# Performance work log

Hardware: AMD Instinct MI355X
Metric: run time of the kernel (lower is better)

The kernel has to match this reference:

```python
import jax, jax.numpy as jnp
import numpy as np

ALPHA = 0.3

def setup_inputs() -> dict:
    key = jax.random.key(0)
    k1, k2, k3, k4 = jax.random.split(key, 4)
    bz, sl, n_pos = 64, 1024, 50
    a_arc = jax.random.normal(k1, (bz, sl, sl), dtype=jnp.float32)
    s_arc = jax.random.normal(k2, (bz, sl, sl), dtype=jnp.float32)
    adds = jax.random.randint(k3, (bz, sl), 0, n_pos, dtype=jnp.int32)
    pos = jax.random.randint(k4, (bz, sl), 0, n_pos, dtype=jnp.int32)
    return {"a_arc": a_arc, "s_arc": s_arc, "adds": adds, "pos": pos, "n_pos": n_pos}


def reference(a_arc, s_arc, adds, pos, n_pos):
    # Bin index for every (head, dep) pair: bin = adds[b,i]*n_pos + adds[b,j]
    bins_add = adds[:, :, None] * n_pos + adds[:, None, :]          # [bz, sl, sl] int32
    # Histogram: sum a_arc values per POS-pair bin (replaces the O(n_pos^2) masked loop)
    score_arc = jax.ops.segment_sum(
        a_arc.reshape(-1), bins_add.reshape(-1), num_segments=n_pos * n_pos)
    score_arc = jax.nn.sigmoid(score_arc)                            # [n_pos^2]
    # Broadcast the binned scores back onto s_arc via the pos-pair bins
    bins_pos = pos[:, :, None] * n_pos + pos[:, None, :]             # [bz, sl, sl]
    return s_arc + ALPHA * score_arc[bins_pos]
```

## Files before the change

### kernel.cpp

```cpp
#include <hip/hip_runtime.h>

constexpr int NPOS  = 50;
constexpr int NBINS = NPOS * NPOS;
constexpr int SL    = 1024;
constexpr int BZ    = 64;
constexpr float ALPHA = 0.3f;

constexpr int NRNG      = 8;
constexpr int PSLICE    = 352;
constexpr int H_THREADS = 256;
constexpr int H_BLOCKS  = BZ * NRNG;

__device__ __forceinline__ int rng_lo(int r) { return r < 2 ? 7 * r : 14 + 6 * (r - 2); }
__device__ __forceinline__ int rng_sz(int r) { return r < 2 ? 7 : 6; }

constexpr int R2_THREADS = 256;
constexpr int R2_BLOCKS  = (NBINS + R2_THREADS - 1) / R2_THREADS;
constexpr int A_THREADS      = 256;
constexpr int ROWS_PER_BLOCK = 32;
constexpr int BLOCKS_PER_B   = SL / ROWS_PER_BLOCK;
constexpr int A_BLOCKS       = BZ * BLOCKS_PER_B;

__global__ __launch_bounds__(H_THREADS) void hist_gather(
    const float* __restrict__ a, const int* __restrict__ adds,
    float* __restrict__ g_part) {
  __shared__ int   adds_s[SL];
  __shared__ float accL[8][SL];
  __shared__ int   list[SL + 8];
  __shared__ int   order2[SL];
  __shared__ int   cnt8[8], off8[8];
  __shared__ int   cntQ[NPOS], offQs[NPOS], offQm[NPOS];
  __shared__ int   nrows_s;

  const int tid = threadIdx.x;
  const int b   = blockIdx.x / NRNG;
  const int rg  = blockIdx.x % NRNG;
  const int lo  = rng_lo(rg), sz = rng_sz(rg);

  ((int4*)adds_s)[tid] = ((const int4*)(adds + (size_t)b * SL))[tid];
  #pragma unroll
  for (int p = 0; p < 8; ++p) ((float4*)&accL[p][0])[tid] = float4{0, 0, 0, 0};
  if (tid < 8) cnt8[tid] = 0;
  if (tid < NPOS) cntQ[tid] = 0;
  __syncthreads();

  for (int i = tid; i < SL; i += H_THREADS) {
    const int p = adds_s[i];
    const int pl = p - lo;
    if ((unsigned)pl < (unsigned)sz) atomicAdd(&cnt8[pl], 1);
    atomicAdd(&cntQ[p], 1);
  }
  __syncthreads();
  if (tid == 0) {
    int run = 0;
    #pragma unroll
    for (int c = 0; c < 8; ++c) { off8[c] = run; run += cnt8[c]; }
    nrows_s = run;
  } else if (tid == 64) {
    int run = 0;
    for (int c = 0; c < NPOS; ++c) { offQs[c] = run; offQm[c] = run; run += cntQ[c]; }
  }
  __syncthreads();
  for (int i = tid; i < SL; i += H_THREADS) {
    const int p = adds_s[i];
    const int pl = p - lo;
    if ((unsigned)pl < (unsigned)sz)
      list[atomicAdd(&off8[pl], 1)] = (pl << 12) | i;
    order2[atomicAdd(&offQm[p], 1)] = i;
  }
  __syncthreads();
  const int N    = nrows_s;
  const int Npad = (N + 7) & ~7;
  if (tid < 8 && N + tid < Npad)
    list[N + tid] = (7 << 12) | (N > 0 ? (list[N - 1] & 0xFFF) : 0);
  __syncthreads();

  const float4* __restrict__ Ab = (const float4*)(a + (size_t)b * SL * SL);
  float4 creg = {0, 0, 0, 0};
  int pcur = 7;

  int    eA[8], eB[8];
  float4 vA[8], vB[8];
  auto loadbank = [&](int (&e)[8], float4 (&v)[8], int k) {
    #pragma unroll
    for (int u = 0; u < 8; ++u) {
      e[u] = __builtin_amdgcn_readfirstlane(list[k + u]);
      v[u] = Ab[(size_t)(e[u] & 0xFFF) * (SL / 4) + tid];
    }
  };
  auto procbank = [&](int (&e)[8], float4 (&v)[8]) {
    #pragma unroll
    for (int u = 0; u < 8; ++u) {
      const int pl = e[u] >> 12;
      if (pl != pcur) {
        ((float4*)&accL[pcur][0])[tid] = creg;
        creg = float4{0, 0, 0, 0};
        pcur = pl;
      }
      creg.x += v[u].x; creg.y += v[u].y; creg.z += v[u].z; creg.w += v[u].w;
    }
  };

  if (Npad > 0) {
    pcur = list[0] >> 12;
    loadbank(eA, vA, 0);
    for (int k = 0; k < Npad; k += 16) {
      if (k + 8 < Npad) loadbank(eB, vB, k + 8);
      procbank(eA, vA);
      if (k + 16 < Npad) loadbank(eA, vA, k + 16);
      if (k + 8 < Npad) procbank(eB, vB);
    }
    ((float4*)&accL[pcur][0])[tid] = creg;
  }
  __syncthreads();

  float* __restrict__ gp = g_part + (size_t)blockIdx.x * PSLICE;
  for (int bin = tid; bin < sz * NPOS; bin += H_THREADS) {
    const int pl = bin / NPOS, q = bin % NPOS;
    const int s0 = offQs[q], n = cntQ[q];
    float s = 0.0f;
    for (int k2 = 0; k2 < n; ++k2) s += accL[pl][order2[s0 + k2]];
    gp[bin] = s;
  }
}

__global__ __launch_bounds__(R2_THREADS) void reduce2(
    const float* __restrict__ g_part, float* __restrict__ g_hist) {
  const int bin = blockIdx.x * R2_THREADS + threadIdx.x;
  if (bin >= NBINS) return;
  const int p = bin / NPOS, q = bin % NPOS;
  const int rg = (p < 14) ? p / 7 : 2 + (p - 14) / 6;
  const int pl = (p < 14) ? p % 7 : (p - 14) % 6;
  float s = 0.0f;
  #pragma unroll 8
  for (int bb = 0; bb < BZ; ++bb)
    s += g_part[(size_t)(bb * NRNG + rg) * PSLICE + pl * NPOS + q];
  g_hist[bin] = s;
}

__global__ __launch_bounds__(A_THREADS) void apply_kernel(
    const float* __restrict__ s, const int* __restrict__ pos,
    const float* __restrict__ g_hist, float* __restrict__ out) {
  __shared__ float sig[NBINS];
  __shared__ int   pos_s[SL];

  const int tid = threadIdx.x;
  const int b   = blockIdx.x / BLOCKS_PER_B;
  const int i0  = (blockIdx.x % BLOCKS_PER_B) * ROWS_PER_BLOCK;

  ((int4*)pos_s)[tid] = ((const int4*)(pos + (size_t)b * SL))[tid];
  for (int k = tid; k < NBINS; k += A_THREADS) {
    const float h = g_hist[k];
    sig[k] = 1.0f / (1.0f + __expf(-h));
  }
  __syncthreads();

  const int4 pj = ((const int4*)pos_s)[tid];
  const size_t rowoff = ((size_t)b * SL + i0) * SL;
  const float4* __restrict__ srow = (const float4*)(s + rowoff);
  float4* __restrict__ orow = (float4*)(out + rowoff);

  for (int r = 0; r < ROWS_PER_BLOCK; ++r) {
    const int base = pos_s[i0 + r] * NPOS;
    const float4 sv = srow[(size_t)r * (SL / 4) + tid];
    float4 ov;
    ov.x = sv.x + ALPHA * sig[base + pj.x];
    ov.y = sv.y + ALPHA * sig[base + pj.y];
    ov.z = sv.z + ALPHA * sig[base + pj.z];
    ov.w = sv.w + ALPHA * sig[base + pj.w];
    orow[(size_t)r * (SL / 4) + tid] = ov;
  }
}

extern "C" void kernel_launch(void* const* d_in, const int* in_sizes, int n_in,
                              void* d_out, int out_size, void* d_ws, size_t ws_size,
                              hipStream_t stream) {
  const float* a_arc = (const float*)d_in[0];
  const float* s_arc = (const float*)d_in[1];
  const int*   adds  = (const int*)d_in[2];
  const int*   pos   = (const int*)d_in[3];
  float* out    = (float*)d_out;
  float* g_hist = (float*)d_ws;
  float* g_part = g_hist + 4096;

  hist_gather <<<H_BLOCKS, H_THREADS, 0, stream>>>(a_arc, adds, g_part);
  reduce2     <<<R2_BLOCKS, R2_THREADS, 0, stream>>>(g_part, g_hist);
  apply_kernel<<<A_BLOCKS, A_THREADS, 0, stream>>>(s_arc, pos, g_hist, out);
}
```

Before: 180.5 us.

## Split histogram gather into 4-POS ranges and row halves with register accumulators

The histogram kernel now uses 13 ranges of 4 POS values and splits each batch's rows into two halves, launching 1664 blocks instead of 512. Each thread accumulates into four named float4 registers instead of flushing a running sum to LDS whenever the POS tag changes. Shared memory per block drops, which allows more resident blocks. In exchange, reduce2 must sum twice as many partial slices, and each block still recomputes the full q-ordering of the sequence, which is now repeated across more blocks.

After: 210.2 us. +16.4%, slower.

```diff
diff --git a/kernel.cpp b/kernel.cpp
--- a/kernel.cpp
+++ b/kernel.cpp
@@ -6,15 +6,13 @@
 constexpr int BZ    = 64;
 constexpr float ALPHA = 0.3f;
 
-constexpr int NRNG      = 8;
-constexpr int PSLICE    = 352;
+constexpr int NRNG      = 13;
+constexpr int SPLITS    = 2;
+constexpr int PSLICE    = 208;
 constexpr int H_THREADS = 256;
-constexpr int H_BLOCKS  = BZ * NRNG;
+constexpr int H_BLOCKS  = BZ * NRNG * SPLITS;
 
-__device__ __forceinline__ int rng_lo(int r) { return r < 2 ? 7 * r : 14 + 6 * (r - 2); }
-__device__ __forceinline__ int rng_sz(int r) { return r < 2 ? 7 : 6; }
-
-constexpr int R2_THREADS = 256;
+constexpr int R2_THREADS = 64;
 constexpr int R2_BLOCKS  = (NBINS + R2_THREADS - 1) / R2_THREADS;
 constexpr int A_THREADS      = 256;
 constexpr int ROWS_PER_BLOCK = 32;
@@ -25,49 +23,50 @@
     const float* __restrict__ a, const int* __restrict__ adds,
     float* __restrict__ g_part) {
   __shared__ int   adds_s[SL];
-  __shared__ float accL[8][SL];
-  __shared__ int   list[SL + 8];
+  __shared__ float accL[4][SL];
+  __shared__ int   list[512 + 8];
   __shared__ int   order2[SL];
-  __shared__ int   cnt8[8], off8[8];
+  __shared__ int   cnt4[4], off4[4];
   __shared__ int   cntQ[NPOS], offQs[NPOS], offQm[NPOS];
   __shared__ int   nrows_s;
 
-  const int tid = threadIdx.x;
-  const int b   = blockIdx.x / NRNG;
-  const int rg  = blockIdx.x % NRNG;
-  const int lo  = rng_lo(rg), sz = rng_sz(rg);
+  const int tid  = threadIdx.x;
+  const int b    = blockIdx.x / (NRNG * SPLITS);
+  const int rem  = blockIdx.x % (NRNG * SPLITS);
+  const int rg   = rem >> 1;
+  const int half = rem & 1;
+  const int lo   = rg * 4;
+  const int sz   = (lo + 4 <= NPOS) ? 4 : (NPOS - lo);
+  const int r0   = half * (SL / SPLITS);
 
   ((int4*)adds_s)[tid] = ((const int4*)(adds + (size_t)b * SL))[tid];
-  #pragma unroll
-  for (int p = 0; p < 8; ++p) ((float4*)&accL[p][0])[tid] = float4{0, 0, 0, 0};
-  if (tid < 8) cnt8[tid] = 0;
+  if (tid < 4) cnt4[tid] = 0;
   if (tid < NPOS) cntQ[tid] = 0;
   __syncthreads();
 
-  for (int i = tid; i < SL; i += H_THREADS) {
-    const int p = adds_s[i];
-    const int pl = p - lo;
-    if ((unsigned)pl < (unsigned)sz) atomicAdd(&cnt8[pl], 1);
-    atomicAdd(&cntQ[p], 1);
+  for (int i = tid; i < SL; i += H_THREADS) atomicAdd(&cntQ[adds_s[i]], 1);
+  for (int i = r0 + tid; i < r0 + SL / SPLITS; i += H_THREADS) {
+    const int pl = adds_s[i] - lo;
+    if ((unsigned)pl < (unsigned)sz) atomicAdd(&cnt4[pl], 1);
   }
   __syncthreads();
   if (tid == 0) {
     int run = 0;
     #pragma unroll
-    for (int c = 0; c < 8; ++c) { off8[c] = run; run += cnt8[c]; }
+    for (int c = 0; c < 4; ++c) { off4[c] = run; run += cnt4[c]; }
     nrows_s = run;
   } else if (tid == 64) {
     int run = 0;
     for (int c = 0; c < NPOS; ++c) { offQs[c] = run; offQm[c] = run; run += cntQ[c]; }
   }
   __syncthreads();
-  for (int i = tid; i < SL; i += H_THREADS) {
-    const int p = adds_s[i];
-    const int pl = p - lo;
+  for (int i = r0 + tid; i < r0 + SL / SPLITS; i += H_THREADS) {
+    const int pl = adds_s[i] - lo;
     if ((unsigned)pl < (unsigned)sz)
-      list[atomicAdd(&off8[pl], 1)] = (pl << 12) | i;
-    order2[atomicAdd(&offQm[p], 1)] = i;
+      list[atomicAdd(&off4[pl], 1)] = (pl << 12) | i;
   }
+  for (int i = tid; i < SL; i += H_THREADS)
+    order2[atomicAdd(&offQm[adds_s[i]], 1)] = i;
   __syncthreads();
   const int N    = nrows_s;
   const int Npad = (N + 7) & ~7;
@@ -76,8 +75,17 @@
   __syncthreads();
 
   const float4* __restrict__ Ab = (const float4*)(a + (size_t)b * SL * SL);
-  float4 creg = {0, 0, 0, 0};
-  int pcur = 7;
+  float4 a0{0,0,0,0}, a1{0,0,0,0}, a2{0,0,0,0}, a3{0,0,0,0}, ad{0,0,0,0};
+
+  auto addto = [&](int pl, const float4& v) {
+    if (pl < 2) {
+      if (pl == 0) { a0.x += v.x; a0.y += v.y; a0.z += v.z; a0.w += v.w; }
+      else         { a1.x += v.x; a1.y += v.y; a1.z += v.z; a1.w += v.w; }
+    } else if (pl < 4) {
+      if (pl == 2) { a2.x += v.x; a2.y += v.y; a2.z += v.z; a2.w += v.w; }
+      else         { a3.x += v.x; a3.y += v.y; a3.z += v.z; a3.w += v.w; }
+    } else         { ad.x += v.x; ad.y += v.y; ad.z += v.z; ad.w += v.w; }
+  };
 
   int    eA[8], eB[8];
   float4 vA[8], vB[8];
@@ -90,19 +98,10 @@
   };
   auto procbank = [&](int (&e)[8], float4 (&v)[8]) {
     #pragma unroll
-    for (int u = 0; u < 8; ++u) {
-      const int pl = e[u] >> 12;
-      if (pl != pcur) {
-        ((float4*)&accL[pcur][0])[tid] = creg;
-        creg = float4{0, 0, 0, 0};
-        pcur = pl;
-      }
-      creg.x += v[u].x; creg.y += v[u].y; creg.z += v[u].z; creg.w += v[u].w;
-    }
+    for (int u = 0; u < 8; ++u) addto(e[u] >> 12, v[u]);
   };
 
   if (Npad > 0) {
-    pcur = list[0] >> 12;
     loadbank(eA, vA, 0);
     for (int k = 0; k < Npad; k += 16) {
       if (k + 8 < Npad) loadbank(eB, vB, k + 8);
@@ -110,8 +109,12 @@
       if (k + 16 < Npad) loadbank(eA, vA, k + 16);
       if (k + 8 < Npad) procbank(eB, vB);
     }
-    ((float4*)&accL[pcur][0])[tid] = creg;
   }
+
+  ((float4*)&accL[0][0])[tid] = a0;
+  ((float4*)&accL[1][0])[tid] = a1;
+  ((float4*)&accL[2][0])[tid] = a2;
+  ((float4*)&accL[3][0])[tid] = a3;
   __syncthreads();
 
   float* __restrict__ gp = g_part + (size_t)blockIdx.x * PSLICE;
@@ -129,12 +132,15 @@
   const int bin = blockIdx.x * R2_THREADS + threadIdx.x;
   if (bin >= NBINS) return;
   const int p = bin / NPOS, q = bin % NPOS;
-  const int rg = (p < 14) ? p / 7 : 2 + (p - 14) / 6;
-  const int pl = (p < 14) ? p % 7 : (p - 14) % 6;
+  const int rg = p >> 2, pl = p & 3;
+  const float* __restrict__ base =
+      g_part + (size_t)(rg * SPLITS) * PSLICE + pl * NPOS + q;
   float s = 0.0f;
-  #pragma unroll 8
-  for (int bb = 0; bb < BZ; ++bb)
-    s += g_part[(size_t)(bb * NRNG + rg) * PSLICE + pl * NPOS + q];
+  #pragma unroll 4
+  for (int bb = 0; bb < BZ; ++bb) {
+    const size_t o = (size_t)bb * (NRNG * SPLITS) * PSLICE;
+    s += base[o] + base[o + PSLICE];
+  }
   g_hist[bin] = s;
 }
 
```
